# Kernel tuning notes

Hardware: AMD Instinct MI355X
Metric: run time of the kernel (lower is better)

The kernel has to match this reference:

```python
import jax, jax.numpy as jnp
import numpy as np

N = 100000   # total nodes across batched graphs
E = 1600000  # total edges
B = 128      # number of graphs in batch
FEAT, H1, H2, P, OUT = 6, 128, 512, 2, 100
M0, M1 = 1024, 512  # MLP hidden dims
BN_EPS = 1e-5


def _lin_init(key, fan_in, fan_out):
    return jax.random.normal(key, (fan_in, fan_out), jnp.float32) / np.sqrt(fan_in)


def setup_inputs() -> dict:
    key = jax.random.key(0)
    ks = jax.random.split(key, 12)
    feat = jax.random.normal(ks[0], (N, FEAT), jnp.float32)
    prompt = jax.random.normal(ks[1], (B, P), jnp.float32)
    src = jax.random.randint(ks[2], (E,), 0, N, jnp.int32)
    dst = jax.random.randint(ks[3], (E,), 0, N, jnp.int32)
    graph_ids = jnp.sort(jax.random.randint(ks[4], (N,), 0, B, jnp.int32))
    return {
        "feat": feat, "prompt": prompt,
        "src": src, "dst": dst, "graph_ids": graph_ids,
        "W0": _lin_init(ks[5], FEAT, H1), "b0": jnp.zeros((H1,), jnp.float32),
        "W1": _lin_init(ks[6], H1, H2), "b1": jnp.zeros((H2,), jnp.float32),
        "Wp": _lin_init(ks[7], P, P), "bp": jnp.zeros((P,), jnp.float32),
        "Wm0": _lin_init(ks[8], H2 + P, M0), "bm0": jnp.zeros((M0,), jnp.float32),
        "g0": jnp.ones((M0,), jnp.float32), "be0": jnp.zeros((M0,), jnp.float32),
        "Wm1": _lin_init(ks[9], M0, M1), "bm1": jnp.zeros((M1,), jnp.float32),
        "g1": jnp.ones((M1,), jnp.float32), "be1": jnp.zeros((M1,), jnp.float32),
        "Wm2": _lin_init(ks[10], M1, OUT), "bm2": jnp.zeros((OUT,), jnp.float32),
    }


def reference(feat, prompt, src, dst, graph_ids,
              W0, b0, W1, b1, Wp, bp,
              Wm0, bm0, g0, be0, Wm1, bm1, g1, be1, Wm2, bm2):
    # GIN layer: neigh = sum_{j in N(i)} h_j ; h' = relu(Linear((1+eps)*h + neigh)), eps=0
    def gin(h, W, b):
        neigh = jax.ops.segment_sum(h[src], dst, num_segments=N)  # gather + scatter-add
        return jax.nn.relu((h + neigh) @ W + b)

    h = gin(feat, W0, b0)   # [N, 128]
    h = gin(h, W1, b1)      # [N, 512]

    pooled = jax.ops.segment_sum(h, graph_ids, num_segments=B)  # dgl.sum_nodes -> [B, 512]
    pr = prompt @ Wp + bp                                        # prompt_nn -> [B, 2]
    x = jnp.concatenate([pooled, pr], axis=-1)                   # [B, 514]

    # MLPBlock mode='NAD': Linear -> BatchNorm1d (batch stats) -> ReLU -> (Dropout p=0)
    def bn(z, g, be):
        m = z.mean(axis=0)
        v = z.var(axis=0)
        return g * (z - m) * jax.lax.rsqrt(v + BN_EPS) + be

    x = jax.nn.relu(bn(x @ Wm0 + bm0, g0, be0))
    x = jax.nn.relu(bn(x @ Wm1 + bm1, g1, be1))
    return x @ Wm2 + bm2  # [B, 100] XANES spectrum
```

## Files before the change

### kernel.cpp

```cpp
#include <hip/hip_runtime.h>
#include <hip/hip_bf16.h>

#define Nn 100000
#define Ee 1600000
#define Bb 128
#define XD 514
#define BN_EPS 1e-5f
#define SCAN_NB 196
#define NPART 8
#define PART_NODES 12500
#define PART_BLKS 2048
#define KC 128

using bf16x8 = __attribute__((ext_vector_type(8))) short;
using f32x4  = __attribute__((ext_vector_type(4))) float;

static __device__ __forceinline__ float grp32_sum(float v){
  v += __shfl_xor(v, 1);
  v += __shfl_xor(v, 2);
  v += __shfl_xor(v, 4);
  v += __shfl_xor(v, 8);
  v += __shfl_xor(v, 16);
  return v;
}

static __device__ __forceinline__ unsigned short f2bf(float f){
  unsigned u = __builtin_bit_cast(unsigned, f);
  unsigned r = (u + 0x7fffu + ((u >> 16) & 1u)) >> 16;
  return (unsigned short)r;
}

static __device__ __forceinline__ float bfl(unsigned u){ return __builtin_bit_cast(float, u << 16); }
static __device__ __forceinline__ float bfh(unsigned u){ return __builtin_bit_cast(float, u & 0xffff0000u); }

__global__ __launch_bounds__(256) void k_count(const int* __restrict__ dst, int* __restrict__ deg){
  int part = blockIdx.x & (NPART-1);
  int lo = part * PART_NODES, hi = lo + PART_NODES;
  int nch = gridDim.x >> 3;
  int chunk = blockIdx.x >> 3;
  for (int e = chunk*256 + threadIdx.x; e < Ee; e += nch*256){
    int d = dst[e];
    if (d >= lo && d < hi) atomicAdd(&deg[d], 1);
  }
}

__global__ __launch_bounds__(256) void k_scanA(const int* __restrict__ deg, int* __restrict__ bsum){
  __shared__ int red[256];
  int b = blockIdx.x, t = threadIdx.x;
  int i0 = b*512 + t;
  int v = 0;
  if (i0 < Nn) v += deg[i0];
  if (i0 + 256 < Nn) v += deg[i0+256];
  red[t] = v; __syncthreads();
  for (int off=128; off>0; off>>=1){
    if (t < off) red[t] += red[t+off];
    __syncthreads();
  }
  if (t==0) bsum[b] = red[0];
}

__global__ __launch_bounds__(256) void k_scanB(const int* __restrict__ bsum, int* __restrict__ boff,
                                               int* __restrict__ rowptrN, int nb){
  __shared__ int sA[256], sB[256];
  int t = threadIdx.x;
  int own = (t < nb) ? bsum[t] : 0;
  sA[t] = own; __syncthreads();
  int* s = sA; int* d = sB;
  #pragma unroll
  for (int off=1; off<256; off<<=1){
    int x = s[t]; if (t>=off) x += s[t-off];
    d[t] = x; __syncthreads();
    int* tmp = s; s = d; d = tmp;
  }
  int incl = s[t];
  if (t < nb) boff[t] = incl - own;
  if (t == 255) *rowptrN = incl;
}

__global__ __launch_bounds__(256) void k_scanC(const int* __restrict__ deg, const int* __restrict__ boff,
                                               int* __restrict__ rowptr){
  __shared__ int sA[256], sB[256];
  int b = blockIdx.x, t = threadIdx.x;
  int i0 = b*512 + 2*t;
  int a = (i0 < Nn) ? deg[i0] : 0;
  int c = (i0+1 < Nn) ? deg[i0+1] : 0;
  int s0 = a + c;
  sA[t] = s0; __syncthreads();
  int* s = sA; int* d = sB;
  #pragma unroll
  for (int off=1; off<256; off<<=1){
    int x = s[t]; if (t>=off) x += s[t-off];
    d[t] = x; __syncthreads();
    int* tmp = s; s = d; d = tmp;
  }
  int excl = s[t] - s0 + boff[b];
  if (i0 < Nn)   rowptr[i0]   = excl;
  if (i0+1 < Nn) rowptr[i0+1] = excl + a;
}

__global__ __launch_bounds__(256) void k_fill(const int* __restrict__ src, const int* __restrict__ dst,
                                              int* __restrict__ cur, int* __restrict__ eidx){
  int part = blockIdx.x & (NPART-1);
  int lo = part * PART_NODES, hi = lo + PART_NODES;
  int nch = gridDim.x >> 3;
  int chunk = blockIdx.x >> 3;
  for (int e = chunk*256 + threadIdx.x; e < Ee; e += nch*256){
    int d = dst[e];
    if (d >= lo && d < hi){
      int p = atomicAdd(&cur[d], 1);
      eidx[p] = src[e];
    }
  }
}

__global__ __launch_bounds__(256) void k_gin1(const float* __restrict__ feat, const int* __restrict__ rowptr,
                                              const int* __restrict__ eidx, float* __restrict__ x1){
  int i = blockIdx.x*256 + threadIdx.x;
  if (i >= Nn) return;
  float a0=feat[i*6+0], a1=feat[i*6+1], a2=feat[i*6+2],
        a3=feat[i*6+3], a4=feat[i*6+4], a5=feat[i*6+5];
  int beg = rowptr[i], end = rowptr[i+1];
  for (int j=beg; j<end; ++j){
    const float* f = feat + eidx[j]*6;
    a0+=f[0]; a1+=f[1]; a2+=f[2]; a3+=f[3]; a4+=f[4]; a5+=f[5];
  }
  float* o = x1 + i*6;
  o[0]=a0; o[1]=a1; o[2]=a2; o[3]=a3; o[4]=a4; o[5]=a5;
}

__global__ __launch_bounds__(256) void k_gin1mlp(const float* __restrict__ x1, const float* __restrict__ W0,
                                                 const float* __restrict__ b0, unsigned short* __restrict__ h1){
  __shared__ float sW[768];
  __shared__ float sb[128];
  int t = threadIdx.x;
  for (int i=t; i<768; i+=256) sW[i] = W0[i];
  if (t < 128) sb[t] = b0[t];
  __syncthreads();
  int row = blockIdx.x*2 + (t>>7);
  int c = t & 127;
  if (row >= Nn) return;
  const float* xr = x1 + row*6;
  float acc = sb[c];
  #pragma unroll
  for (int f=0; f<6; ++f) acc += xr[f]*sW[f*128+c];
  h1[row*128+c] = f2bf(fmaxf(acc, 0.f));
}

__global__ __launch_bounds__(256) void k_gather2(const unsigned short* __restrict__ h1,
                                                 const int* __restrict__ rowptr,
                                                 const int* __restrict__ eidx,
                                                 unsigned short* __restrict__ xb){
  int gt = blockIdx.x*256 + threadIdx.x;
  int node = gt >> 4;
  if (node >= Nn) return;
  int l = threadIdx.x & 15;
  int off = l*8;
  float a0,a1,a2,a3,a4,a5,a6,a7;
  {
    uint4 v = *(const uint4*)&h1[(size_t)node*128 + off];
    a0=bfl(v.x); a1=bfh(v.x); a2=bfl(v.y); a3=bfh(v.y);
    a4=bfl(v.z); a5=bfh(v.z); a6=bfl(v.w); a7=bfh(v.w);
  }
  int beg = rowptr[node], end = rowptr[node+1];
  int j = beg;
  for (; j+1 < end; j += 2){
    int s0 = eidx[j], s1 = eidx[j+1];
    uint4 u = *(const uint4*)&h1[(size_t)s0*128 + off];
    uint4 w = *(const uint4*)&h1[(size_t)s1*128 + off];
    a0 += bfl(u.x) + bfl(w.x);
    a1 += bfh(u.x) + bfh(w.x);
    a2 += bfl(u.y) + bfl(w.y);
    a3 += bfh(u.y) + bfh(w.y);
    a4 += bfl(u.z) + bfl(w.z);
    a5 += bfh(u.z) + bfh(w.z);
    a6 += bfl(u.w) + bfl(w.w);
    a7 += bfh(u.w) + bfh(w.w);
  }
  if (j < end){
    uint4 u = *(const uint4*)&h1[(size_t)eidx[j]*128 + off];
    a0 += bfl(u.x); a1 += bfh(u.x);
    a2 += bfl(u.y); a3 += bfh(u.y);
    a4 += bfl(u.z); a5 += bfh(u.z);
    a6 += bfl(u.w); a7 += bfh(u.w);
  }
  uint4 o;
  o.x = (unsigned)f2bf(a0) | ((unsigned)f2bf(a1) << 16);
  o.y = (unsigned)f2bf(a2) | ((unsigned)f2bf(a3) << 16);
  o.z = (unsigned)f2bf(a4) | ((unsigned)f2bf(a5) << 16);
  o.w = (unsigned)f2bf(a6) | ((unsigned)f2bf(a7) << 16);
  *(uint4*)&xb[(size_t)node*128 + off] = o;
}

__global__ __launch_bounds__(256) void k_packW(const float* __restrict__ W1, unsigned short* __restrict__ W1p){
  int t = blockIdx.x*256 + threadIdx.x;
  int l = t & 63;
  int s = (t >> 6) & 3;
  int f = t >> 8;
  int n = f*16 + (l & 15);
  int kb = s*32 + (l >> 4)*8;
  unsigned short o[8];
  #pragma unroll
  for (int e=0; e<8; ++e) o[e] = f2bf(W1[(kb+e)*512 + n]);
  uint4 pk;
  pk.x = (unsigned)o[0] | ((unsigned)o[1] << 16);
  pk.y = (unsigned)o[2] | ((unsigned)o[3] << 16);
  pk.z = (unsigned)o[4] | ((unsigned)o[5] << 16);
  pk.w = (unsigned)o[6] | ((unsigned)o[7] << 16);
  *(uint4*)&W1p[t*8] = pk;
}

__global__ __launch_bounds__(256) void k_gin2m(const unsigned short* __restrict__ xb,
                                               const unsigned short* __restrict__ W1p,
                                               const float* __restrict__ b1,
                                               const int* __restrict__ gids,
                                               float* __restrict__ pool){
  __shared__ float pool_lds[4][128];
  __shared__ int wgid[4];
  __shared__ int wuni_s[4];
  int w = threadIdx.x >> 6, l = threadIdx.x & 63;
  int wrow = blockIdx.x*128 + w*32;
  int fbase = blockIdx.y * 8;
  int kbase = (l >> 4) * 8;

  bf16x8 a[2][4];
  #pragma unroll
  for (int r=0; r<2; ++r){
    int arow = wrow + r*16 + (l & 15);
    if (arow > Nn-1) arow = Nn-1;
    const bf16x8* ap = (const bf16x8*)&xb[(size_t)arow*128 + kbase];
    #pragma unroll
    for (int s=0; s<4; ++s) a[r][s] = ap[s*4];
  }

  bool wvalid = wrow < Nn;
  bool wuni = (wrow + 31 < Nn) && (gids[wrow] == gids[wrow + 31]);
  if (l == 0){ wgid[w] = wuni ? gids[wrow] : -1; wuni_s[w] = wuni ? 1 : 0; }

  int rb[2], g0[2];
  bool uval[2];
  #pragma unroll
  for (int r=0; r<2; ++r){
    rb[r] = wrow + r*16 + ((l >> 4) & 3)*4;
    int i0 = rb[r], i3 = rb[r]+3;
    int c0 = i0 < Nn ? i0 : Nn-1;
    int c3 = i3 < Nn ? i3 : Nn-1;
    g0[r] = gids[c0];
    int g3 = gids[c3];
    uval[r] = (i3 < Nn) && (g0[r] == g3);
  }

  float acc_pool[8];
  #pragma unroll
  for (int i=0; i<8; ++i) acc_pool[i] = 0.f;

  const bf16x8* BpAll = (const bf16x8*)W1p;
  bf16x8 bcur[4];
  #pragma unroll
  for (int s=0; s<4; ++s) bcur[s] = BpAll[(fbase*4 + s)*64 + l];

  #pragma unroll
  for (int fi=0; fi<8; ++fi){
    int f = fbase + fi;
    bf16x8 bnext[4];
    if (fi < 7){
      #pragma unroll
      for (int s=0; s<4; ++s) bnext[s] = BpAll[((f+1)*4 + s)*64 + l];
    }
    f32x4 acc0 = {0.f,0.f,0.f,0.f};
    f32x4 acc1 = {0.f,0.f,0.f,0.f};
    #pragma unroll
    for (int s=0; s<4; ++s){
      acc0 = __builtin_amdgcn_mfma_f32_16x16x32_bf16(a[0][s], bcur[s], acc0, 0, 0, 0);
      acc1 = __builtin_amdgcn_mfma_f32_16x16x32_bf16(a[1][s], bcur[s], acc1, 0, 0, 0);
    }
    int col = f*16 + (l & 15);
    float bc = b1[col];
    if (wuni){
      float vsum = 0.f;
      #pragma unroll
      for (int r=0; r<2; ++r){
        f32x4 acc = r ? acc1 : acc0;
        float v = fmaxf(acc[0]+bc, 0.f) + fmaxf(acc[1]+bc, 0.f)
                + fmaxf(acc[2]+bc, 0.f) + fmaxf(acc[3]+bc, 0.f);
        v += __shfl_xor(v, 16);
        v += __shfl_xor(v, 32);
        vsum += v;
      }
      acc_pool[fi] = vsum;
    } else if (wvalid){
      #pragma unroll
      for (int r=0; r<2; ++r){
        f32x4 acc = r ? acc1 : acc0;
        float y0 = fmaxf(acc[0] + bc, 0.f);
        float y1 = fmaxf(acc[1] + bc, 0.f);
        float y2 = fmaxf(acc[2] + bc, 0.f);
        float y3 = fmaxf(acc[3] + bc, 0.f);
        int gg = g0[r];
        int ok = uval[r] ? 1 : 0;
        float v = y0 + y1 + y2 + y3;
        int gX  = __shfl_xor(gg, 16);
        int okX = __shfl_xor(ok, 16);
        ok = ok & okX & (gg == gX ? 1 : 0);
        float v2 = v + __shfl_xor(v, 16);
        int gY  = __shfl_xor(gg, 32);
        int okY = __shfl_xor(ok, 32);
        float v4 = v2 + __shfl_xor(v2, 32);
        ok = ok & okY & (gg == gY ? 1 : 0);
        if (ok){
          if (l < 16) atomicAdd(&pool[gg*XD + col], v4);
        } else {
          int base = rb[r];
          if (base   < Nn) atomicAdd(&pool[gids[base  ]*XD + col], y0);
          if (base+1 < Nn) atomicAdd(&pool[gids[base+1]*XD + col], y1);
          if (base+2 < Nn) atomicAdd(&pool[gids[base+2]*XD + col], y2);
          if (base+3 < Nn) atomicAdd(&pool[gids[base+3]*XD + col], y3);
        }
      }
    }
    if (fi < 7){
      #pragma unroll
      for (int s=0; s<4; ++s) bcur[s] = bnext[s];
    }
  }

  if (wuni && l < 16){
    #pragma unroll
    for (int fi=0; fi<8; ++fi) pool_lds[w][fi*16 + l] = acc_pool[fi];
  }
  __syncthreads();
  int t = threadIdx.x;
  if (t < 128){
    int cg = -1; float s = 0.f;
    #pragma unroll
    for (int ww=0; ww<4; ++ww){
      if (!wuni_s[ww]) continue;
      int g = wgid[ww];
      if (g != cg){
        if (cg >= 0) atomicAdd(&pool[cg*XD + fbase*16 + t], s);
        cg = g; s = 0.f;
      }
      s += pool_lds[ww][t];
    }
    if (cg >= 0) atomicAdd(&pool[cg*XD + fbase*16 + t], s);
  }
}

__global__ void k_pr(const float* __restrict__ prompt, const float* __restrict__ Wp,
                     const float* __restrict__ bp, float* __restrict__ xmlp){
  int t = threadIdx.x;
  if (t < 256){
    int r = t>>1, j = t&1;
    float v = prompt[r*2+0]*Wp[0*2+j] + prompt[r*2+1]*Wp[1*2+j] + bp[j];
    xmlp[r*XD + 512 + j] = v;
  }
}

__global__ __launch_bounds__(256) void k_lin(const float* __restrict__ X, const float* __restrict__ W,
                                             float* __restrict__ Zp, int K, int NC){
  __shared__ float xT[16][KC];
  int c = blockIdx.x*256 + threadIdx.x;
  int row0 = blockIdx.y*16;
  int k0 = blockIdx.z*KC;
  int kn = K - k0; if (kn > KC) kn = KC;
  if (kn == KC){
    int r = threadIdx.x >> 7;
    int kk = threadIdx.x & 127;
    #pragma unroll
    for (int i=0; i<8; ++i) xT[r + i*2][kk] = X[(size_t)(row0 + r + i*2)*K + k0 + kk];
  } else {
    for (int idx = threadIdx.x; idx < 16*kn; idx += 256){
      int r = idx / kn, kk = idx - r*kn;
      xT[r][kk] = X[(size_t)(row0+r)*K + k0 + kk];
    }
  }
  __syncthreads();
  float acc[16];
  #pragma unroll
  for (int r=0; r<16; ++r) acc[r] = 0.f;
  for (int kk=0; kk<kn; ++kk){
    float w = W[(size_t)(k0+kk)*NC + c];
    #pragma unroll
    for (int r=0; r<16; ++r) acc[r] += xT[r][kk]*w;
  }
  float* Zb = Zp + (size_t)blockIdx.z*128*NC;
  #pragma unroll
  for (int r=0; r<16; ++r) Zb[(size_t)(row0+r)*NC + c] = acc[r];
}

__global__ __launch_bounds__(256) void k_bnrelu(const float* __restrict__ Zp, const float* __restrict__ bias,
                                                const float* __restrict__ gamma, const float* __restrict__ beta,
                                                float* __restrict__ Y, int NC, int nk){
  int grp = threadIdx.x>>5, l32 = threadIdx.x&31;
  int col = blockIdx.x*8 + grp;
  int r0 = l32*4;
  float z0=0.f, z1=0.f, z2=0.f, z3=0.f;
  for (int j=0; j<nk; ++j){
    const float* Zb = Zp + (size_t)j*128*NC + col;
    z0 += Zb[(size_t)(r0+0)*NC];
    z1 += Zb[(size_t)(r0+1)*NC];
    z2 += Zb[(size_t)(r0+2)*NC];
    z3 += Zb[(size_t)(r0+3)*NC];
  }
  float bc = bias[col];
  z0+=bc; z1+=bc; z2+=bc; z3+=bc;
  float mean = grp32_sum(z0+z1+z2+z3) * (1.f/128.f);
  float d0=z0-mean, d1=z1-mean, d2=z2-mean, d3=z3-mean;
  float var = grp32_sum(d0*d0+d1*d1+d2*d2+d3*d3) * (1.f/128.f);
  float sc = gamma[col]*rsqrtf(var + BN_EPS);
  float bt = beta[col];
  Y[(size_t)(r0+0)*NC+col] = fmaxf(d0*sc+bt, 0.f);
  Y[(size_t)(r0+1)*NC+col] = fmaxf(d1*sc+bt, 0.f);
  Y[(size_t)(r0+2)*NC+col] = fmaxf(d2*sc+bt, 0.f);
  Y[(size_t)(r0+3)*NC+col] = fmaxf(d3*sc+bt, 0.f);
}

__global__ __launch_bounds__(128) void k_out(const float* __restrict__ y1, const float* __restrict__ W2,
                                             const float* __restrict__ b2, float* __restrict__ out){
  __shared__ float yr[512];
  int r = blockIdx.x;
  for (int k=threadIdx.x; k<512; k+=128) yr[k] = y1[r*512+k];
  __syncthreads();
  int c = threadIdx.x;
  if (c < 100){
    float a0=0.f, a1=0.f, a2=0.f, a3=0.f;
    for (int k=0; k<512; k+=4){
      a0 += yr[k+0]*W2[(k+0)*100+c];
      a1 += yr[k+1]*W2[(k+1)*100+c];
      a2 += yr[k+2]*W2[(k+2)*100+c];
      a3 += yr[k+3]*W2[(k+3)*100+c];
    }
    out[r*100+c] = b2[c] + ((a0+a1)+(a2+a3));
  }
}

extern "C" void kernel_launch(void* const* d_in, const int* in_sizes, int n_in,
                              void* d_out, int out_size, void* d_ws, size_t ws_size,
                              hipStream_t stream)
{
  const float* feat   = (const float*)d_in[0];
  const float* prompt = (const float*)d_in[1];
  const int*   src    = (const int*)d_in[2];
  const int*   dst    = (const int*)d_in[3];
  const int*   gids   = (const int*)d_in[4];
  const float* W0  = (const float*)d_in[5];
  const float* b0  = (const float*)d_in[6];
  const float* W1  = (const float*)d_in[7];
  const float* b1  = (const float*)d_in[8];
  const float* Wp  = (const float*)d_in[9];
  const float* bp  = (const float*)d_in[10];
  const float* Wm0 = (const float*)d_in[11];
  const float* bm0 = (const float*)d_in[12];
  const float* g0  = (const float*)d_in[13];
  const float* be0 = (const float*)d_in[14];
  const float* Wm1 = (const float*)d_in[15];
  const float* bm1 = (const float*)d_in[16];
  const float* g1  = (const float*)d_in[17];
  const float* be1 = (const float*)d_in[18];
  const float* Wm2 = (const float*)d_in[19];
  const float* bm2 = (const float*)d_in[20];
  float* out = (float*)d_out;

  char* p = (char*)d_ws;
  auto carve = [&](size_t bytes) -> void* {
    void* r = (void*)p;
    p += (bytes + 255) & ~(size_t)255;
    return r;
  };
  int*   deg    = (int*)carve((size_t)Nn*4);
  int*   rowptr = (int*)carve((size_t)(Nn+1)*4);
  int*   cur    = (int*)carve((size_t)Nn*4);
  int*   bsum   = (int*)carve(256*4);
  int*   boff   = (int*)carve(256*4);
  int*   eidx   = (int*)carve((size_t)Ee*4);
  float* x1     = (float*)carve((size_t)Nn*6*4);
  unsigned short* h1  = (unsigned short*)carve((size_t)Nn*128*2);
  unsigned short* xb  = (unsigned short*)carve((size_t)Nn*128*2);
  unsigned short* W1p = (unsigned short*)carve((size_t)128*512*2);
  float* xmlp   = (float*)carve((size_t)Bb*XD*4);
  float* y0     = (float*)carve((size_t)Bb*1024*4);
  float* y1     = (float*)carve((size_t)Bb*512*4);

  float* Zp0 = (float*)eidx;
  float* Zp1 = (float*)x1;

  hipMemsetAsync(deg, 0, (size_t)Nn*4, stream);
  hipMemsetAsync(xmlp, 0, (size_t)Bb*XD*4, stream);

  k_packW<<<32, 256, 0, stream>>>(W1, W1p);

  k_count<<<PART_BLKS, 256, 0, stream>>>(dst, deg);
  k_scanA<<<SCAN_NB, 256, 0, stream>>>(deg, bsum);
  k_scanB<<<1, 256, 0, stream>>>(bsum, boff, rowptr + Nn, SCAN_NB);
  k_scanC<<<SCAN_NB, 256, 0, stream>>>(deg, boff, rowptr);
  hipMemcpyAsync(cur, rowptr, (size_t)Nn*4, hipMemcpyDeviceToDevice, stream);
  k_fill<<<PART_BLKS, 256, 0, stream>>>(src, dst, cur, eidx);

  k_gin1<<<(Nn+255)/256, 256, 0, stream>>>(feat, rowptr, eidx, x1);
  k_gin1mlp<<<Nn/2, 256, 0, stream>>>(x1, W0, b0, h1);

  k_gather2<<<(Nn*16+255)/256, 256, 0, stream>>>(h1, rowptr, eidx, xb);
  dim3 g2((Nn+127)/128, 4);
  k_gin2m<<<g2, 256, 0, stream>>>(xb, W1p, b1, gids, xmlp);

  k_pr<<<1, 256, 0, stream>>>(prompt, Wp, bp, xmlp);

  dim3 gl0(1024/256, 8, (XD + KC - 1)/KC);
  k_lin<<<gl0, 256, 0, stream>>>(xmlp, Wm0, Zp0, XD, 1024);
  k_bnrelu<<<1024/8, 256, 0, stream>>>(Zp0, bm0, g0, be0, y0, 1024, (XD + KC - 1)/KC);

  dim3 gl1(512/256, 8, 1024/KC);
  k_lin<<<gl1, 256, 0, stream>>>(y0, Wm1, Zp1, 1024, 512);
  k_bnrelu<<<512/8, 256, 0, stream>>>(Zp1, bm1, g1, be1, y1, 512, 1024/KC);

  k_out<<<Bb, 128, 0, stream>>>(y1, Wm2, bm2, out);
}
```

Baseline: 496.8 us.

## Pre-bin edges by destination partition before degree count and CSR fill

Adds a binning pass that reads src/dst once, buckets each edge into one of 8 destination partitions using shared-memory histograms, and writes (dst,src) pairs into per-partition regions that reuse the h1 buffer. The count and fill kernels then read only their partition's edges instead of every block scanning all 1.6M edges and filtering by range. This removes the 8x redundant reads of dst/src, at the cost of an extra write and read of an 8-byte-per-edge bin array. It relies on a fixed per-partition capacity (PCAP), which holds for uniformly random dst.

```diff
diff --git a/kernel.cpp b/kernel.cpp
--- a/kernel.cpp
+++ b/kernel.cpp
@@ -11,6 +11,9 @@
 #define PART_NODES 12500
 #define PART_BLKS 2048
 #define KC 128
+#define NBIN_BLKS 2048
+#define CH 784
+#define PCAP 212992
 
 using bf16x8 = __attribute__((ext_vector_type(8))) short;
 using f32x4  = __attribute__((ext_vector_type(4))) float;
@@ -33,14 +36,41 @@
 static __device__ __forceinline__ float bfl(unsigned u){ return __builtin_bit_cast(float, u << 16); }
 static __device__ __forceinline__ float bfh(unsigned u){ return __builtin_bit_cast(float, u & 0xffff0000u); }
 
-__global__ __launch_bounds__(256) void k_count(const int* __restrict__ dst, int* __restrict__ deg){
-  int part = blockIdx.x & (NPART-1);
-  int lo = part * PART_NODES, hi = lo + PART_NODES;
-  int nch = gridDim.x >> 3;
-  int chunk = blockIdx.x >> 3;
-  for (int e = chunk*256 + threadIdx.x; e < Ee; e += nch*256){
-    int d = dst[e];
-    if (d >= lo && d < hi) atomicAdd(&deg[d], 1);
+__global__ __launch_bounds__(256) void k_bin(const int* __restrict__ src, const int* __restrict__ dst,
+                                             int* __restrict__ gCnt, int2* __restrict__ bins){
+  __shared__ int sd[CH], ss[CH];
+  __shared__ int hist[8], wbase[8], roff[8];
+  int t = threadIdx.x;
+  if (t < 8){ hist[t] = 0; roff[t] = 0; }
+  __syncthreads();
+  int e0 = blockIdx.x * CH;
+  int e1 = e0 + CH; if (e1 > Ee) e1 = Ee;
+  int n = e1 - e0;
+  for (int i = t; i < n; i += 256){
+    int d = __builtin_nontemporal_load(&dst[e0 + i]);
+    int s = __builtin_nontemporal_load(&src[e0 + i]);
+    sd[i] = d; ss[i] = s;
+    atomicAdd(&hist[d / PART_NODES], 1);
+  }
+  __syncthreads();
+  if (t < 8) wbase[t] = atomicAdd(&gCnt[t], hist[t]);
+  __syncthreads();
+  for (int i = t; i < n; i += 256){
+    int d = sd[i];
+    int p = d / PART_NODES;
+    int off = atomicAdd(&roff[p], 1);
+    bins[(size_t)p * PCAP + wbase[p] + off] = make_int2(d, ss[i]);
+  }
+}
+
+__global__ __launch_bounds__(256) void k_count2(const int2* __restrict__ bins, const int* __restrict__ gCnt,
+                                                int* __restrict__ deg){
+  int p = blockIdx.x & (NPART-1);
+  int nch = gridDim.x >> 3, chunk = blockIdx.x >> 3;
+  int n = gCnt[p];
+  const int2* bp = bins + (size_t)p * PCAP;
+  for (int i = chunk*256 + threadIdx.x; i < n; i += nch*256){
+    atomicAdd(&deg[bp[i].x], 1);
   }
 }
 
@@ -98,18 +128,16 @@
   if (i0+1 < Nn) rowptr[i0+1] = excl + a;
 }
 
-__global__ __launch_bounds__(256) void k_fill(const int* __restrict__ src, const int* __restrict__ dst,
-                                              int* __restrict__ cur, int* __restrict__ eidx){
-  int part = blockIdx.x & (NPART-1);
-  int lo = part * PART_NODES, hi = lo + PART_NODES;
-  int nch = gridDim.x >> 3;
-  int chunk = blockIdx.x >> 3;
-  for (int e = chunk*256 + threadIdx.x; e < Ee; e += nch*256){
-    int d = dst[e];
-    if (d >= lo && d < hi){
-      int p = atomicAdd(&cur[d], 1);
-      eidx[p] = src[e];
-    }
+__global__ __launch_bounds__(256) void k_fill2(const int2* __restrict__ bins, const int* __restrict__ gCnt,
+                                               int* __restrict__ cur, int* __restrict__ eidx){
+  int p = blockIdx.x & (NPART-1);
+  int nch = gridDim.x >> 3, chunk = blockIdx.x >> 3;
+  int n = gCnt[p];
+  const int2* bp = bins + (size_t)p * PCAP;
+  for (int i = chunk*256 + threadIdx.x; i < n; i += nch*256){
+    int2 e = bp[i];
+    int q = atomicAdd(&cur[e.x], 1);
+    eidx[q] = e.y;
   }
 }
 
@@ -471,6 +499,7 @@
   int*   cur    = (int*)carve((size_t)Nn*4);
   int*   bsum   = (int*)carve(256*4);
   int*   boff   = (int*)carve(256*4);
+  int*   gCnt   = (int*)carve(256*4);
   int*   eidx   = (int*)carve((size_t)Ee*4);
   float* x1     = (float*)carve((size_t)Nn*6*4);
   unsigned short* h1  = (unsigned short*)carve((size_t)Nn*128*2);
@@ -480,20 +509,23 @@
   float* y0     = (float*)carve((size_t)Bb*1024*4);
   float* y1     = (float*)carve((size_t)Bb*512*4);
 
+  int2*  bins = (int2*)h1;
   float* Zp0 = (float*)eidx;
   float* Zp1 = (float*)x1;
 
   hipMemsetAsync(deg, 0, (size_t)Nn*4, stream);
+  hipMemsetAsync(gCnt, 0, 8*4, stream);
   hipMemsetAsync(xmlp, 0, (size_t)Bb*XD*4, stream);
 
   k_packW<<<32, 256, 0, stream>>>(W1, W1p);
 
-  k_count<<<PART_BLKS, 256, 0, stream>>>(dst, deg);
+  k_bin<<<NBIN_BLKS, 256, 0, stream>>>(src, dst, gCnt, bins);
+  k_count2<<<PART_BLKS, 256, 0, stream>>>(bins, gCnt, deg);
   k_scanA<<<SCAN_NB, 256, 0, stream>>>(deg, bsum);
   k_scanB<<<1, 256, 0, stream>>>(bsum, boff, rowptr + Nn, SCAN_NB);
   k_scanC<<<SCAN_NB, 256, 0, stream>>>(deg, boff, rowptr);
   hipMemcpyAsync(cur, rowptr, (size_t)Nn*4, hipMemcpyDeviceToDevice, stream);
-  k_fill<<<PART_BLKS, 256, 0, stream>>>(src, dst, cur, eidx);
+  k_fill2<<<PART_BLKS, 256, 0, stream>>>(bins, gCnt, cur, eidx);
 
   k_gin1<<<(Nn+255)/256, 256, 0, stream>>>(feat, rowptr, eidx, x1);
   k_gin1mlp<<<Nn/2, 256, 0, stream>>>(x1, W0, b0, h1);
```

After: 524.8 us. 5.6% more time.
